# Optimization experiments

Hardware: AMD Instinct MI355X
Metric: run time of the kernel (lower is better)

The kernel has to match this reference:

```python
import jax, jax.numpy as jnp
import numpy as np

B, L, E, H = 2, 2048, 1024, 16
D = E // H

def setup_inputs() -> dict:
    key = jax.random.key(0)
    ks = jax.random.split(key, 6)
    values = jax.random.normal(ks[0], (B, L, E), dtype=jnp.float32)
    keys = jax.random.normal(ks[1], (B, L, E), dtype=jnp.float32)
    query = jax.random.normal(ks[2], (B, L, E), dtype=jnp.float32)
    mask = jax.random.randint(ks[3], (B, 1, L, L), 0, 2, dtype=jnp.int32)
    W_out = jax.random.normal(ks[4], (E, E), dtype=jnp.float32) * 0.02
    b_out = jax.random.normal(ks[5], (E,), dtype=jnp.float32) * 0.02
    return {"values": values, "keys": keys, "query": query, "mask": mask,
            "W_out": W_out, "b_out": b_out}

def reference(values, keys, query, mask, W_out, b_out):
    # Note: source module never applies its per-head q/k/v Linear layers;
    # it only reshapes inputs, so we do the same.
    b, l, e = query.shape
    v = values.reshape(b, l, H, D)   # [B, K, H, D]
    k = keys.reshape(b, l, H, D)     # [B, K, H, D]
    q = query.reshape(b, l, H, D)    # [B, Q, H, D]
    # scores[b,h,q,k] = sum_d q[b,q,h,d] * k[b,k,h,d]
    scores = jnp.einsum('bqhd,bkhd->bhqk', q, k)
    scores = jnp.where(mask == 0, jnp.float32(-1e20), scores)
    # source scales by 1/sqrt(embed_size), not head_dim
    attn = jax.nn.softmax(scores / jnp.float32(E ** 0.5), axis=3)
    out = jnp.einsum('bhqk,bkhd->bqhd', attn, v).reshape(b, l, e)
    out = out @ W_out.T + b_out  # torch Linear: x @ W^T + b
    return out
```

## Files before the change

kernel.cpp:

```cpp
#include <hip/hip_runtime.h>
#include <hip/hip_bf16.h>

typedef __bf16 bf16;
typedef __bf16 bf16x8 __attribute__((ext_vector_type(8)));
typedef __bf16 bf16x4 __attribute__((ext_vector_type(4)));
typedef float  f32x2  __attribute__((ext_vector_type(2)));
typedef float  f32x4  __attribute__((ext_vector_type(4)));
typedef float  f32x16 __attribute__((ext_vector_type(16)));

#define B_ 2
#define L_ 2048
#define E_ 1024
#define H_ 16
#define D_ 64

__device__ __forceinline__ int swz(int r, int c) {
    return r * 64 + (((c ^ (r & 7)) & 7) << 3);
}

#define DMA16(gp, lp)                                                              \
    __builtin_amdgcn_global_load_lds(                                              \
        (const __attribute__((address_space(1))) unsigned int*)(gp),               \
        (__attribute__((address_space(3))) unsigned int*)(lp), 16, 0, 0)

__global__ __launch_bounds__(256) void prep_kernel(const float* __restrict__ v,
                                                   const float* __restrict__ keys,
                                                   const int* __restrict__ mask,
                                                   const float* __restrict__ W,
                                                   bf16* __restrict__ vt_,
                                                   bf16* __restrict__ kt_,
                                                   unsigned int* __restrict__ mtq2,
                                                   bf16* __restrict__ wbt) {
    __shared__ __attribute__((aligned(16))) float tile[64 * 65];
    const int bid = blockIdx.x;
    const int t = threadIdx.x;
    if (bid < 1024) {
        int bh = bid >> 5, b = bh >> 4, h = bh & 15, kt = bid & 31;
        int kk = t >> 2, dg = t & 3;
        const float* src = v + (((size_t)(b * L_ + kt * 64 + kk)) * H_ + h) * D_ + dg * 16;
        float4 f[4];
#pragma unroll
        for (int i = 0; i < 4; i++) f[i] = reinterpret_cast<const float4*>(src)[i];
#pragma unroll
        for (int i = 0; i < 16; i++)
            tile[(dg * 16 + i) * 65 + kk] = reinterpret_cast<const float*>(f)[i];
        __syncthreads();
        int dd = t >> 2, cg = t & 3;
        const int sig[16] = {0, 1, 2, 3, 8, 9, 10, 11, 4, 5, 6, 7, 12, 13, 14, 15};
        bf16 tmp[16];
#pragma unroll
        for (int p = 0; p < 16; p++)
            tmp[p] = (bf16)tile[dd * 65 + cg * 16 + sig[p]];
        bf16* dst = vt_ + ((size_t)bh * 32 + kt) * 4096;
        *reinterpret_cast<uint4*>(dst + swz(dd, cg * 2))     = *reinterpret_cast<const uint4*>(&tmp[0]);
        *reinterpret_cast<uint4*>(dst + swz(dd, cg * 2 + 1)) = *reinterpret_cast<const uint4*>(&tmp[8]);
    } else if (bid < 2048) {
        int idx = bid - 1024;
        int b = idx >> 9;
        int q = (idx & 511) * 4 + (t >> 6);
        int li = t & 63;
        const int* mrow = mask + ((size_t)b * L_ + q) * L_;
        unsigned int* mq = mtq2 + (size_t)b * 64 * 2048;
#pragma unroll 2
        for (int pass = 0; pass < 8; pass++) {
            int4 m4 = reinterpret_cast<const int4*>(mrow)[pass * 64 + li];
            unsigned long long b0 = __ballot(m4.x & 1);
            unsigned long long b1 = __ballot(m4.y & 1);
            unsigned long long b2 = __ballot(m4.z & 1);
            unsigned long long b3 = __ballot(m4.w & 1);
            if (li < 8) {
                unsigned int word = (unsigned int)((b0 >> (8 * li)) & 0xFFull)
                                  | ((unsigned int)((b1 >> (8 * li)) & 0xFFull) << 8)
                                  | ((unsigned int)((b2 >> (8 * li)) & 0xFFull) << 16)
                                  | ((unsigned int)((b3 >> (8 * li)) & 0xFFull) << 24);
                mq[(size_t)(pass * 8 + li) * 2048 + q] = word;
            }
        }
    } else if (bid < 3072) {
        int idx = bid - 2048;
        int b = idx >> 9, h = (idx >> 5) & 15, kt = idx & 31;
        int r = t >> 2, cg = t & 3;
        const float* src = keys + ((size_t)(b * L_ + kt * 64 + r)) * E_ + h * 64 + cg * 16;
        float4 f[4];
#pragma unroll
        for (int i = 0; i < 4; i++) f[i] = reinterpret_cast<const float4*>(src)[i];
        bf16 tmp[16];
#pragma unroll
        for (int i = 0; i < 16; i++)
            tmp[i] = (bf16)reinterpret_cast<const float*>(f)[i];
        bf16* dst = kt_ + ((size_t)(b * 16 + h) * 32 + kt) * 4096;
        *reinterpret_cast<uint4*>(dst + swz(r, cg * 2))     = *reinterpret_cast<const uint4*>(&tmp[0]);
        *reinterpret_cast<uint4*>(dst + swz(r, cg * 2 + 1)) = *reinterpret_cast<const uint4*>(&tmp[8]);
    } else {
        int idx = bid - 3072;
        int n6 = idx >> 4, kt = idx & 15;
        int r = t >> 2, cg = t & 3;
        const float* src = W + ((size_t)(n6 * 64 + r)) * E_ + kt * 64 + cg * 16;
        float4 f[4];
#pragma unroll
        for (int i = 0; i < 4; i++) f[i] = reinterpret_cast<const float4*>(src)[i];
        bf16 tmp[16];
#pragma unroll
        for (int i = 0; i < 16; i++)
            tmp[i] = (bf16)reinterpret_cast<const float*>(f)[i];
        bf16* dst = wbt + ((size_t)(n6 * 16 + kt)) * 4096;
        *reinterpret_cast<uint4*>(dst + swz(r, cg * 2))     = *reinterpret_cast<const uint4*>(&tmp[0]);
        *reinterpret_cast<uint4*>(dst + swz(r, cg * 2 + 1)) = *reinterpret_cast<const uint4*>(&tmp[8]);
    }
}

__global__ __launch_bounds__(256, 4) void attn_kernel(const float* __restrict__ q_,
                                                      const bf16* __restrict__ kt_,
                                                      const bf16* __restrict__ vt_,
                                                      const unsigned int* __restrict__ mtq2,
                                                      bf16* __restrict__ xbt) {
    __shared__ __attribute__((aligned(16))) char smem[40960];
    bf16* Qs = (bf16*)(smem + 32768);
    float* Om = (float*)smem;
    float* Lrow = (float*)(smem + 16384);
    bf16* Xs = (bf16*)(smem + 16896);

    const int bh = blockIdx.y, b = bh >> 4, hd = bh & 15;
    const int q0 = blockIdx.x * 64;
    const int t = threadIdx.x;
    const int w = t >> 6, lane = t & 63, h = lane >> 5, l31 = lane & 31;
    const int wq = w & 1, wk = w >> 1;
    const int r_ = t >> 2, cg = t & 3;

    const float CSCALE = 1.4426950408889634f / 32.0f;

    const bf16* kbase = kt_ + (size_t)bh * 32 * 4096;
    const bf16* vbase = vt_ + (size_t)bh * 32 * 4096;

    {
        const bf16* gk = kbase + w * 1024 + lane * 8;
        DMA16(gk, smem + w * 2048);
        DMA16(gk + 512, smem + w * 2048 + 1024);
        const bf16* gv = vbase + w * 1024 + lane * 8;
        DMA16(gv, smem + 16384 + w * 2048);
        DMA16(gv + 512, smem + 16384 + w * 2048 + 1024);
    }
    {
        const float* src = q_ + ((size_t)(b * L_ + q0 + r_)) * E_ + hd * 64 + cg * 16;
        float4 f[4];
#pragma unroll
        for (int i = 0; i < 4; i++) f[i] = reinterpret_cast<const float4*>(src)[i];
        bf16 tmp[16];
#pragma unroll
        for (int i = 0; i < 16; i++)
            tmp[i] = (bf16)(reinterpret_cast<const float*>(f)[i] * CSCALE);
        *reinterpret_cast<uint4*>(&Qs[swz(r_, cg * 2)])     = *reinterpret_cast<const uint4*>(&tmp[0]);
        *reinterpret_cast<uint4*>(&Qs[swz(r_, cg * 2 + 1)]) = *reinterpret_cast<const uint4*>(&tmp[8]);
    }
    __syncthreads();

    bf16x8 bq[4];
#pragma unroll
    for (int dc = 0; dc < 4; dc++)
        bq[dc] = *reinterpret_cast<const bf16x8*>(&Qs[swz(wq * 32 + l31, dc * 2 + h)]);

    f32x16 oc[2] = {{}, {}};
    f32x2 ls = {0.0f, 0.0f};

    const unsigned int* mbase = mtq2 + (size_t)b * 64 * 2048 + q0 + wq * 32 + l31;
    unsigned int mw = mbase[(size_t)wk * 2048];

    for (int kt = 0; kt < L_ / 64; kt++) {
        __syncthreads();
        bf16* Kc = (bf16*)(smem + (kt & 1) * 8192);
        bf16* Vc = (bf16*)(smem + 16384 + (kt & 1) * 8192);
        if (kt + 1 < L_ / 64) {
            char* Kn = smem + ((kt + 1) & 1) * 8192;
            char* Vn = smem + 16384 + ((kt + 1) & 1) * 8192;
            const bf16* gk = kbase + (size_t)(kt + 1) * 4096 + w * 1024 + lane * 8;
            DMA16(gk, Kn + w * 2048);
            DMA16(gk + 512, Kn + w * 2048 + 1024);
            const bf16* gv = vbase + (size_t)(kt + 1) * 4096 + w * 1024 + lane * 8;
            DMA16(gv, Vn + w * 2048);
            DMA16(gv + 512, Vn + w * 2048 + 1024);
        }
        unsigned int mw_nxt = (kt + 1 < L_ / 64)
                                  ? mbase[(size_t)((kt + 1) * 2 + wk) * 2048] : 0u;

        f32x16 st = {};
        __builtin_amdgcn_s_setprio(1);
#pragma unroll
        for (int dc = 0; dc < 4; dc++) {
            bf16x8 ak = *reinterpret_cast<const bf16x8*>(&Kc[swz(wk * 32 + l31, dc * 2 + h)]);
            st = __builtin_amdgcn_mfma_f32_32x32x16_bf16(ak, bq[dc], st, 0, 0, 0);
        }
        __builtin_amdgcn_s_setprio(0);

        const unsigned int mwh = mw >> h;
        float pv[16];
#pragma unroll
        for (int i = 0; i < 16; i += 2) {
            const int b0 = 8 * (i & 3) + 2 * (i >> 2);
            const int b1 = 8 * ((i + 1) & 3) + 2 * ((i + 1) >> 2);
            float e0 = __builtin_amdgcn_exp2f(st[i]);
            float e1 = __builtin_amdgcn_exp2f(st[i + 1]);
            int m0 = ((int)(mwh << (31 - b0))) >> 31;
            int m1 = ((int)(mwh << (31 - b1))) >> 31;
            pv[i]     = __int_as_float(__float_as_int(e0) & m0);
            pv[i + 1] = __int_as_float(__float_as_int(e1) & m1);
            ls += (f32x2){pv[i], pv[i + 1]};
        }
        bf16x8 bp[2];
#pragma unroll
        for (int kc = 0; kc < 2; kc++)
#pragma unroll
            for (int j = 0; j < 8; j++)
                bp[kc][j] = (bf16)pv[kc * 8 + j];

        __builtin_amdgcn_s_setprio(1);
#pragma unroll
        for (int da = 0; da < 2; da++)
#pragma unroll
            for (int kc = 0; kc < 2; kc++) {
                bf16x8 av = *reinterpret_cast<const bf16x8*>(&Vc[swz(da * 32 + l31, wk * 4 + kc * 2 + h)]);
                oc[da] = __builtin_amdgcn_mfma_f32_32x32x16_bf16(av, bp[kc], oc[da], 0, 0, 0);
            }
        __builtin_amdgcn_s_setprio(0);
        mw = mw_nxt;
    }
    __syncthreads();

    float lsum = ls.x + ls.y;
    float lw = lsum + __shfl(lsum, lane ^ 32, 64);
    if (wk == 1) {
#pragma unroll
        for (int da = 0; da < 2; da++)
#pragma unroll
            for (int i = 0; i < 16; i++) {
                int d = da * 32 + (i & 3) + 8 * (i >> 2) + 4 * h;
                Om[d * 64 + wq * 32 + l31] = oc[da][i];
            }
        if (h == 0) Lrow[wq * 32 + l31] = lw;
    }
    __syncthreads();
    if (wk == 0) {
        float rinv = 1.0f / (lw + Lrow[wq * 32 + l31]);
#pragma unroll
        for (int da = 0; da < 2; da++)
#pragma unroll
            for (int g = 0; g < 4; g++) {
                int d0 = da * 32 + 8 * g + 4 * h;
                bf16x4 pk;
#pragma unroll
                for (int r = 0; r < 4; r++)
                    pk[r] = (bf16)((oc[da][g * 4 + r] + Om[(d0 + r) * 64 + wq * 32 + l31]) * rinv);
                *reinterpret_cast<bf16x4*>(&Xs[(wq * 32 + l31) * 72 + d0]) = pk;
            }
    }
    __syncthreads();
    {
        bf16* xtile = xbt + ((size_t)((b * 32 + (q0 >> 6)) * 16 + hd)) * 4096;
        *reinterpret_cast<uint4*>(xtile + swz(r_, cg * 2))     = *reinterpret_cast<const uint4*>(&Xs[r_ * 72 + cg * 16]);
        *reinterpret_cast<uint4*>(xtile + swz(r_, cg * 2 + 1)) = *reinterpret_cast<const uint4*>(&Xs[r_ * 72 + cg * 16 + 8]);
    }
}

__global__ __launch_bounds__(256, 3) void proj_kernel(const bf16* __restrict__ xbt,
                                                      const bf16* __restrict__ wbt,
                                                      const float* __restrict__ bias,
                                                      float* __restrict__ out) {
    __shared__ __attribute__((aligned(16))) char smem[49152];
    const int n0 = blockIdx.x * 64, m0 = blockIdx.y * 128;
    const int t = threadIdx.x;
    const int w = t >> 6, lane = t & 63, h = lane >> 5, l31 = lane & 31;
    const int wm = w >> 1, wn = w & 1;

    const bf16* a0 = xbt + ((size_t)(m0 >> 6)) * 16 * 4096;
    const bf16* a1 = a0 + 16 * 4096;
    const bf16* bb_ = wbt + ((size_t)(n0 >> 6)) * 16 * 4096;

    {
#pragma unroll
        for (int i = 0; i < 4; i++) {
            int c = w * 4 + i;
            const bf16* g = ((c >> 3) ? a1 : a0) + (c & 7) * 512 + lane * 8;
            DMA16(g, smem + c * 1024);
        }
#pragma unroll
        for (int i = 0; i < 2; i++) {
            int c = w * 2 + i;
            DMA16(bb_ + c * 512 + lane * 8, smem + 32768 + c * 1024);
        }
    }

    f32x16 acc[2] = {{}, {}};
    for (int kt = 0; kt < E_ / 64; kt++) {
        __syncthreads();
        bf16* Ac = (bf16*)(smem + (kt & 1) * 16384);
        bf16* Bc = (bf16*)(smem + 32768 + (kt & 1) * 8192);
        if (kt + 1 < E_ / 64) {
            char* An = smem + ((kt + 1) & 1) * 16384;
            char* Bn = smem + 32768 + ((kt + 1) & 1) * 8192;
            const bf16* an0 = a0 + (kt + 1) * 4096;
            const bf16* an1 = a1 + (kt + 1) * 4096;
            const bf16* bn = bb_ + (kt + 1) * 4096;
#pragma unroll
            for (int i = 0; i < 4; i++) {
                int c = w * 4 + i;
                const bf16* g = ((c >> 3) ? an1 : an0) + (c & 7) * 512 + lane * 8;
                DMA16(g, An + c * 1024);
            }
#pragma unroll
            for (int i = 0; i < 2; i++) {
                int c = w * 2 + i;
                DMA16(bn + c * 512 + lane * 8, Bn + c * 1024);
            }
        }
#pragma unroll
        for (int dc = 0; dc < 4; dc++) {
            bf16x8 bfr = *reinterpret_cast<const bf16x8*>(&Bc[swz(wn * 32 + l31, dc * 2 + h)]);
#pragma unroll
            for (int mi = 0; mi < 2; mi++) {
                bf16x8 afr = *reinterpret_cast<const bf16x8*>(&Ac[wm * 4096 + swz(mi * 32 + l31, dc * 2 + h)]);
                acc[mi] = __builtin_amdgcn_mfma_f32_32x32x16_bf16(afr, bfr, acc[mi], 0, 0, 0);
            }
        }
    }

    float bv = bias[n0 + wn * 32 + l31];
#pragma unroll
    for (int mi = 0; mi < 2; mi++)
#pragma unroll
        for (int i = 0; i < 16; i++) {
            int row = m0 + wm * 64 + mi * 32 + (i & 3) + 8 * (i >> 2) + 4 * h;
            out[(size_t)row * E_ + n0 + wn * 32 + l31] = acc[mi][i] + bv;
        }
}

extern "C" void kernel_launch(void* const* d_in, const int* in_sizes, int n_in,
                              void* d_out, int out_size, void* d_ws, size_t ws_size,
                              hipStream_t stream) {
    (void)in_sizes; (void)n_in; (void)out_size; (void)ws_size;
    const float* values = (const float*)d_in[0];
    const float* keys   = (const float*)d_in[1];
    const float* query  = (const float*)d_in[2];
    const int*   mask   = (const int*)d_in[3];
    const float* W_out  = (const float*)d_in[4];
    const float* b_out  = (const float*)d_in[5];
    float* out = (float*)d_out;

    char* ws = (char*)d_ws;
    bf16* vt_ = (bf16*)(ws);
    bf16* kt_ = (bf16*)(ws + 8388608);
    bf16* wbt = (bf16*)(ws + 16777216);
    unsigned int* mtq2 = (unsigned int*)(ws + 18874368);
    bf16* xbt = (bf16*)(ws + 19922944);

    prep_kernel<<<3328, 256, 0, stream>>>(values, keys, mask, W_out, vt_, kt_, mtq2, wbt);
    attn_kernel<<<dim3(L_ / 64, B_ * H_), 256, 0, stream>>>(query, kt_, vt_, mtq2, xbt);
    proj_kernel<<<dim3(E_ / 64, (B_ * L_) / 128), 256, 0, stream>>>(xbt, wbt, b_out, out);
}
```

Baseline: 191.6 us.

## Software-pipeline QK^T of the next tile with PV of the previous tile

Restructures the attention loop so each iteration issues the QK^T MFMAs for key tile kt together with the PV MFMAs for tile kt-1, with a peeled prologue and epilogue. V tiles move to triple buffering, reusing the Q staging area once Q is in registers. The goal is to hide the exp/mask/convert latency between the two matmuls behind independent MFMA work. The grid is also transposed so consecutive blocks cover different heads at the same query tile, which changes cache locality. The cost is more live registers (preloaded K and V fragments plus the carried score tile), which may pressure occupancy at the launch bound of 4.

```diff
diff --git a/kernel.cpp b/kernel.cpp
--- a/kernel.cpp
+++ b/kernel.cpp
@@ -120,8 +120,8 @@
     float* Lrow = (float*)(smem + 16384);
     bf16* Xs = (bf16*)(smem + 16896);
 
-    const int bh = blockIdx.y, b = bh >> 4, hd = bh & 15;
-    const int q0 = blockIdx.x * 64;
+    const int bh = blockIdx.x, b = bh >> 4, hd = bh & 15;
+    const int q0 = blockIdx.y * 64;
     const int t = threadIdx.x;
     const int w = t >> 6, lane = t & 63, h = lane >> 5, l31 = lane & 31;
     const int wq = w & 1, wk = w >> 1;
@@ -159,39 +159,59 @@
     for (int dc = 0; dc < 4; dc++)
         bq[dc] = *reinterpret_cast<const bf16x8*>(&Qs[swz(wq * 32 + l31, dc * 2 + h)]);
 
+    {
+        const bf16* gk = kbase + 4096 + w * 1024 + lane * 8;
+        DMA16(gk, smem + 8192 + w * 2048);
+        DMA16(gk + 512, smem + 8192 + w * 2048 + 1024);
+        const bf16* gv = vbase + 4096 + w * 1024 + lane * 8;
+        DMA16(gv, smem + 24576 + w * 2048);
+        DMA16(gv + 512, smem + 24576 + w * 2048 + 1024);
+    }
+
+    const unsigned int* mbase = mtq2 + (size_t)b * 64 * 2048 + q0 + wq * 32 + l31;
+    unsigned int mwHeld = mbase[(size_t)wk * 2048];
+
     f32x16 oc[2] = {{}, {}};
     f32x2 ls = {0.0f, 0.0f};
 
-    const unsigned int* mbase = mtq2 + (size_t)b * 64 * 2048 + q0 + wq * 32 + l31;
-    unsigned int mw = mbase[(size_t)wk * 2048];
-
-    for (int kt = 0; kt < L_ / 64; kt++) {
-        __syncthreads();
-        bf16* Kc = (bf16*)(smem + (kt & 1) * 8192);
-        bf16* Vc = (bf16*)(smem + 16384 + (kt & 1) * 8192);
-        if (kt + 1 < L_ / 64) {
-            char* Kn = smem + ((kt + 1) & 1) * 8192;
-            char* Vn = smem + 16384 + ((kt + 1) & 1) * 8192;
-            const bf16* gk = kbase + (size_t)(kt + 1) * 4096 + w * 1024 + lane * 8;
-            DMA16(gk, Kn + w * 2048);
-            DMA16(gk + 512, Kn + w * 2048 + 1024);
-            const bf16* gv = vbase + (size_t)(kt + 1) * 4096 + w * 1024 + lane * 8;
-            DMA16(gv, Vn + w * 2048);
-            DMA16(gv + 512, Vn + w * 2048 + 1024);
-        }
-        unsigned int mw_nxt = (kt + 1 < L_ / 64)
-                                  ? mbase[(size_t)((kt + 1) * 2 + wk) * 2048] : 0u;
-
-        f32x16 st = {};
-        __builtin_amdgcn_s_setprio(1);
+    f32x16 st = {};
+    {
+        const bf16* Kc = (const bf16*)smem;
 #pragma unroll
         for (int dc = 0; dc < 4; dc++) {
             bf16x8 ak = *reinterpret_cast<const bf16x8*>(&Kc[swz(wk * 32 + l31, dc * 2 + h)]);
             st = __builtin_amdgcn_mfma_f32_32x32x16_bf16(ak, bq[dc], st, 0, 0, 0);
         }
-        __builtin_amdgcn_s_setprio(0);
-
-        const unsigned int mwh = mw >> h;
+    }
+
+    int vP = 16384, vC = 24576, vN = 32768;
+    for (int kt = 1; kt < L_ / 64; kt++) {
+        __syncthreads();
+        const int koff = (kt & 1) << 13;
+        if (kt + 1 < L_ / 64) {
+            const int koffN = koff ^ 8192;
+            const bf16* gk = kbase + (size_t)(kt + 1) * 4096 + w * 1024 + lane * 8;
+            DMA16(gk, smem + koffN + w * 2048);
+            DMA16(gk + 512, smem + koffN + w * 2048 + 1024);
+            const bf16* gv = vbase + (size_t)(kt + 1) * 4096 + w * 1024 + lane * 8;
+            DMA16(gv, smem + vN + w * 2048);
+            DMA16(gv + 512, smem + vN + w * 2048 + 1024);
+        }
+        unsigned int mwN = mbase[(size_t)(kt * 2 + wk) * 2048];
+
+        const bf16* Kc = (const bf16*)(smem + koff);
+        const bf16* Vp = (const bf16*)(smem + vP);
+        bf16x8 ak[4], av[4];
+#pragma unroll
+        for (int dc = 0; dc < 4; dc++)
+            ak[dc] = *reinterpret_cast<const bf16x8*>(&Kc[swz(wk * 32 + l31, dc * 2 + h)]);
+#pragma unroll
+        for (int j = 0; j < 4; j++) {
+            const int da = j >> 1, kc = j & 1;
+            av[j] = *reinterpret_cast<const bf16x8*>(&Vp[swz(da * 32 + l31, wk * 4 + kc * 2 + h)]);
+        }
+
+        const unsigned int mwh = mwHeld >> h;
         float pv[16];
 #pragma unroll
         for (int i = 0; i < 16; i += 2) {
@@ -213,15 +233,49 @@
                 bp[kc][j] = (bf16)pv[kc * 8 + j];
 
         __builtin_amdgcn_s_setprio(1);
-#pragma unroll
-        for (int da = 0; da < 2; da++)
-#pragma unroll
-            for (int kc = 0; kc < 2; kc++) {
-                bf16x8 av = *reinterpret_cast<const bf16x8*>(&Vc[swz(da * 32 + l31, wk * 4 + kc * 2 + h)]);
-                oc[da] = __builtin_amdgcn_mfma_f32_32x32x16_bf16(av, bp[kc], oc[da], 0, 0, 0);
-            }
+        st = (f32x16){};
+#pragma unroll
+        for (int dc = 0; dc < 4; dc++)
+            st = __builtin_amdgcn_mfma_f32_32x32x16_bf16(ak[dc], bq[dc], st, 0, 0, 0);
+#pragma unroll
+        for (int j = 0; j < 4; j++) {
+            const int da = j >> 1, kc = j & 1;
+            oc[da] = __builtin_amdgcn_mfma_f32_32x32x16_bf16(av[j], bp[kc], oc[da], 0, 0, 0);
+        }
         __builtin_amdgcn_s_setprio(0);
-        mw = mw_nxt;
+
+        mwHeld = mwN;
+        int tmpv = vP; vP = vC; vC = vN; vN = tmpv;
+    }
+
+    {
+        const unsigned int mwh = mwHeld >> h;
+        float pv[16];
+#pragma unroll
+        for (int i = 0; i < 16; i += 2) {
+            const int b0 = 8 * (i & 3) + 2 * (i >> 2);
+            const int b1 = 8 * ((i + 1) & 3) + 2 * ((i + 1) >> 2);
+            float e0 = __builtin_amdgcn_exp2f(st[i]);
+            float e1 = __builtin_amdgcn_exp2f(st[i + 1]);
+            int m0 = ((int)(mwh << (31 - b0))) >> 31;
+            int m1 = ((int)(mwh << (31 - b1))) >> 31;
+            pv[i]     = __int_as_float(__float_as_int(e0) & m0);
+            pv[i + 1] = __int_as_float(__float_as_int(e1) & m1);
+            ls += (f32x2){pv[i], pv[i + 1]};
+        }
+        bf16x8 bp[2];
+#pragma unroll
+        for (int kc = 0; kc < 2; kc++)
+#pragma unroll
+            for (int j = 0; j < 8; j++)
+                bp[kc][j] = (bf16)pv[kc * 8 + j];
+        const bf16* Vp = (const bf16*)(smem + vP);
+#pragma unroll
+        for (int j = 0; j < 4; j++) {
+            const int da = j >> 1, kc = j & 1;
+            bf16x8 av = *reinterpret_cast<const bf16x8*>(&Vp[swz(da * 32 + l31, wk * 4 + kc * 2 + h)]);
+            oc[da] = __builtin_amdgcn_mfma_f32_32x32x16_bf16(av, bp[kc], oc[da], 0, 0, 0);
+        }
     }
     __syncthreads();
 
@@ -352,6 +406,6 @@
     bf16* xbt = (bf16*)(ws + 19922944);
 
     prep_kernel<<<3328, 256, 0, stream>>>(values, keys, mask, W_out, vt_, kt_, mtq2, wbt);
-    attn_kernel<<<dim3(L_ / 64, B_ * H_), 256, 0, stream>>>(query, kt_, vt_, mtq2, xbt);
+    attn_kernel<<<dim3(B_ * H_, L_ / 64), 256, 0, stream>>>(query, kt_, vt_, mtq2, xbt);
     proj_kernel<<<dim3(E_ / 64, (B_ * L_) / 128), 256, 0, stream>>>(xbt, wbt, b_out, out);
 }
```

Result: no change. 195.3 us (+1.9%).

## Halve attention block to two waves, each covering all 64 queries

Applied to the files above, without the earlier changes.

The attention kernel now runs with 128 threads (2 waves) instead of 4. Each wave handles one 32-key half of every tile for all 64 queries. K and V fragments are loaded from LDS once per tile and reused across two query halves, which doubles the MFMA work per LDS read and halves the waves that sync on each barrier. The mask word is now loaded in the same iteration rather than prefetched. The cost is roughly twice the accumulator registers per wave and fewer waves per block to hide latency.

```diff
diff --git a/kernel.cpp b/kernel.cpp
--- a/kernel.cpp
+++ b/kernel.cpp
@@ -109,7 +109,7 @@
     }
 }
 
-__global__ __launch_bounds__(256, 4) void attn_kernel(const float* __restrict__ q_,
+__global__ __launch_bounds__(128, 2) void attn_kernel(const float* __restrict__ q_,
                                                       const bf16* __restrict__ kt_,
                                                       const bf16* __restrict__ vt_,
                                                       const unsigned int* __restrict__ mtq2,
@@ -124,8 +124,7 @@
     const int q0 = blockIdx.x * 64;
     const int t = threadIdx.x;
     const int w = t >> 6, lane = t & 63, h = lane >> 5, l31 = lane & 31;
-    const int wq = w & 1, wk = w >> 1;
-    const int r_ = t >> 2, cg = t & 3;
+    const int r_ = t >> 1, half = t & 1;
 
     const float CSCALE = 1.4426950408889634f / 32.0f;
 
@@ -133,130 +132,163 @@
     const bf16* vbase = vt_ + (size_t)bh * 32 * 4096;
 
     {
-        const bf16* gk = kbase + w * 1024 + lane * 8;
-        DMA16(gk, smem + w * 2048);
-        DMA16(gk + 512, smem + w * 2048 + 1024);
-        const bf16* gv = vbase + w * 1024 + lane * 8;
-        DMA16(gv, smem + 16384 + w * 2048);
-        DMA16(gv + 512, smem + 16384 + w * 2048 + 1024);
+        const bf16* gk = kbase + w * 2048 + lane * 8;
+        const bf16* gv = vbase + w * 2048 + lane * 8;
+#pragma unroll
+        for (int i = 0; i < 4; i++) {
+            DMA16(gk + i * 512, smem + w * 4096 + i * 1024);
+            DMA16(gv + i * 512, smem + 16384 + w * 4096 + i * 1024);
+        }
     }
     {
-        const float* src = q_ + ((size_t)(b * L_ + q0 + r_)) * E_ + hd * 64 + cg * 16;
-        float4 f[4];
-#pragma unroll
-        for (int i = 0; i < 4; i++) f[i] = reinterpret_cast<const float4*>(src)[i];
-        bf16 tmp[16];
-#pragma unroll
-        for (int i = 0; i < 16; i++)
+        const float* src = q_ + ((size_t)(b * L_ + q0 + r_)) * E_ + hd * 64 + half * 32;
+        float4 f[8];
+#pragma unroll
+        for (int i = 0; i < 8; i++) f[i] = reinterpret_cast<const float4*>(src)[i];
+        bf16 tmp[32];
+#pragma unroll
+        for (int i = 0; i < 32; i++)
             tmp[i] = (bf16)(reinterpret_cast<const float*>(f)[i] * CSCALE);
-        *reinterpret_cast<uint4*>(&Qs[swz(r_, cg * 2)])     = *reinterpret_cast<const uint4*>(&tmp[0]);
-        *reinterpret_cast<uint4*>(&Qs[swz(r_, cg * 2 + 1)]) = *reinterpret_cast<const uint4*>(&tmp[8]);
+#pragma unroll
+        for (int j = 0; j < 4; j++)
+            *reinterpret_cast<uint4*>(&Qs[swz(r_, half * 4 + j)]) =
+                *reinterpret_cast<const uint4*>(&tmp[j * 8]);
     }
     __syncthreads();
 
-    bf16x8 bq[4];
-#pragma unroll
-    for (int dc = 0; dc < 4; dc++)
-        bq[dc] = *reinterpret_cast<const bf16x8*>(&Qs[swz(wq * 32 + l31, dc * 2 + h)]);
-
-    f32x16 oc[2] = {{}, {}};
-    f32x2 ls = {0.0f, 0.0f};
-
-    const unsigned int* mbase = mtq2 + (size_t)b * 64 * 2048 + q0 + wq * 32 + l31;
-    unsigned int mw = mbase[(size_t)wk * 2048];
+    bf16x8 bq[2][4];
+#pragma unroll
+    for (int qh = 0; qh < 2; qh++)
+#pragma unroll
+        for (int dc = 0; dc < 4; dc++)
+            bq[qh][dc] = *reinterpret_cast<const bf16x8*>(&Qs[swz(qh * 32 + l31, dc * 2 + h)]);
+
+    f32x16 oc[2][2] = {{{}, {}}, {{}, {}}};
+    f32x2 ls[2] = {{0.0f, 0.0f}, {0.0f, 0.0f}};
+
+    const unsigned int* mbase = mtq2 + (size_t)b * 64 * 2048 + q0 + l31;
 
     for (int kt = 0; kt < L_ / 64; kt++) {
         __syncthreads();
-        bf16* Kc = (bf16*)(smem + (kt & 1) * 8192);
-        bf16* Vc = (bf16*)(smem + 16384 + (kt & 1) * 8192);
+        const bf16* Kc = (const bf16*)(smem + (kt & 1) * 8192);
+        const bf16* Vc = (const bf16*)(smem + 16384 + (kt & 1) * 8192);
         if (kt + 1 < L_ / 64) {
-            char* Kn = smem + ((kt + 1) & 1) * 8192;
-            char* Vn = smem + 16384 + ((kt + 1) & 1) * 8192;
-            const bf16* gk = kbase + (size_t)(kt + 1) * 4096 + w * 1024 + lane * 8;
-            DMA16(gk, Kn + w * 2048);
-            DMA16(gk + 512, Kn + w * 2048 + 1024);
-            const bf16* gv = vbase + (size_t)(kt + 1) * 4096 + w * 1024 + lane * 8;
-            DMA16(gv, Vn + w * 2048);
-            DMA16(gv + 512, Vn + w * 2048 + 1024);
-        }
-        unsigned int mw_nxt = (kt + 1 < L_ / 64)
-                                  ? mbase[(size_t)((kt + 1) * 2 + wk) * 2048] : 0u;
-
-        f32x16 st = {};
+            char* Kn = smem + ((kt + 1) & 1) * 8192 + w * 4096;
+            char* Vn = smem + 16384 + ((kt + 1) & 1) * 8192 + w * 4096;
+            const bf16* gk = kbase + (size_t)(kt + 1) * 4096 + w * 2048 + lane * 8;
+            const bf16* gv = vbase + (size_t)(kt + 1) * 4096 + w * 2048 + lane * 8;
+#pragma unroll
+            for (int i = 0; i < 4; i++) {
+                DMA16(gk + i * 512, Kn + i * 1024);
+                DMA16(gv + i * 512, Vn + i * 1024);
+            }
+        }
+        unsigned int mw0 = mbase[(size_t)(kt * 2 + w) * 2048];
+        unsigned int mw1 = mbase[(size_t)(kt * 2 + w) * 2048 + 32];
+
+        bf16x8 ak[4], av[4];
+#pragma unroll
+        for (int dc = 0; dc < 4; dc++)
+            ak[dc] = *reinterpret_cast<const bf16x8*>(&Kc[swz(w * 32 + l31, dc * 2 + h)]);
+#pragma unroll
+        for (int j = 0; j < 4; j++) {
+            const int da = j >> 1, kc = j & 1;
+            av[j] = *reinterpret_cast<const bf16x8*>(&Vc[swz(da * 32 + l31, w * 4 + kc * 2 + h)]);
+        }
+
+        f32x16 st[2] = {{}, {}};
         __builtin_amdgcn_s_setprio(1);
 #pragma unroll
         for (int dc = 0; dc < 4; dc++) {
-            bf16x8 ak = *reinterpret_cast<const bf16x8*>(&Kc[swz(wk * 32 + l31, dc * 2 + h)]);
-            st = __builtin_amdgcn_mfma_f32_32x32x16_bf16(ak, bq[dc], st, 0, 0, 0);
+            st[0] = __builtin_amdgcn_mfma_f32_32x32x16_bf16(ak[dc], bq[0][dc], st[0], 0, 0, 0);
+            st[1] = __builtin_amdgcn_mfma_f32_32x32x16_bf16(ak[dc], bq[1][dc], st[1], 0, 0, 0);
         }
         __builtin_amdgcn_s_setprio(0);
 
-        const unsigned int mwh = mw >> h;
-        float pv[16];
-#pragma unroll
-        for (int i = 0; i < 16; i += 2) {
-            const int b0 = 8 * (i & 3) + 2 * (i >> 2);
-            const int b1 = 8 * ((i + 1) & 3) + 2 * ((i + 1) >> 2);
-            float e0 = __builtin_amdgcn_exp2f(st[i]);
-            float e1 = __builtin_amdgcn_exp2f(st[i + 1]);
-            int m0 = ((int)(mwh << (31 - b0))) >> 31;
-            int m1 = ((int)(mwh << (31 - b1))) >> 31;
-            pv[i]     = __int_as_float(__float_as_int(e0) & m0);
-            pv[i + 1] = __int_as_float(__float_as_int(e1) & m1);
-            ls += (f32x2){pv[i], pv[i + 1]};
-        }
-        bf16x8 bp[2];
-#pragma unroll
-        for (int kc = 0; kc < 2; kc++)
-#pragma unroll
-            for (int j = 0; j < 8; j++)
-                bp[kc][j] = (bf16)pv[kc * 8 + j];
+        bf16x8 bp[2][2];
+#pragma unroll
+        for (int qh = 0; qh < 2; qh++) {
+            const unsigned int mwh = (qh ? mw1 : mw0) >> h;
+            float pv[16];
+#pragma unroll
+            for (int i = 0; i < 16; i += 2) {
+                const int b0 = 8 * (i & 3) + 2 * (i >> 2);
+                const int b1 = 8 * ((i + 1) & 3) + 2 * ((i + 1) >> 2);
+                float e0 = __builtin_amdgcn_exp2f(st[qh][i]);
+                float e1 = __builtin_amdgcn_exp2f(st[qh][i + 1]);
+                int m0 = ((int)(mwh << (31 - b0))) >> 31;
+                int m1 = ((int)(mwh << (31 - b1))) >> 31;
+                pv[i]     = __int_as_float(__float_as_int(e0) & m0);
+                pv[i + 1] = __int_as_float(__float_as_int(e1) & m1);
+                ls[qh] += (f32x2){pv[i], pv[i + 1]};
+            }
+#pragma unroll
+            for (int kc = 0; kc < 2; kc++)
+#pragma unroll
+                for (int j = 0; j < 8; j++)
+                    bp[qh][kc][j] = (bf16)pv[kc * 8 + j];
+        }
 
         __builtin_amdgcn_s_setprio(1);
 #pragma unroll
         for (int da = 0; da < 2; da++)
 #pragma unroll
             for (int kc = 0; kc < 2; kc++) {
-                bf16x8 av = *reinterpret_cast<const bf16x8*>(&Vc[swz(da * 32 + l31, wk * 4 + kc * 2 + h)]);
-                oc[da] = __builtin_amdgcn_mfma_f32_32x32x16_bf16(av, bp[kc], oc[da], 0, 0, 0);
+                oc[0][da] = __builtin_amdgcn_mfma_f32_32x32x16_bf16(av[da * 2 + kc], bp[0][kc], oc[0][da], 0, 0, 0);
+                oc[1][da] = __builtin_amdgcn_mfma_f32_32x32x16_bf16(av[da * 2 + kc], bp[1][kc], oc[1][da], 0, 0, 0);
             }
         __builtin_amdgcn_s_setprio(0);
-        mw = mw_nxt;
     }
     __syncthreads();
 
-    float lsum = ls.x + ls.y;
-    float lw = lsum + __shfl(lsum, lane ^ 32, 64);
-    if (wk == 1) {
-#pragma unroll
-        for (int da = 0; da < 2; da++)
-#pragma unroll
-            for (int i = 0; i < 16; i++) {
-                int d = da * 32 + (i & 3) + 8 * (i >> 2) + 4 * h;
-                Om[d * 64 + wq * 32 + l31] = oc[da][i];
-            }
-        if (h == 0) Lrow[wq * 32 + l31] = lw;
+    float lw[2];
+#pragma unroll
+    for (int qh = 0; qh < 2; qh++) {
+        float s = ls[qh].x + ls[qh].y;
+        lw[qh] = s + __shfl(s, lane ^ 32, 64);
+    }
+    if (w == 1) {
+#pragma unroll
+        for (int qh = 0; qh < 2; qh++)
+#pragma unroll
+            for (int da = 0; da < 2; da++)
+#pragma unroll
+                for (int i = 0; i < 16; i++) {
+                    int d = da * 32 + (i & 3) + 8 * (i >> 2) + 4 * h;
+                    Om[d * 64 + qh * 32 + l31] = oc[qh][da][i];
+                }
+        if (h == 0) {
+            Lrow[l31] = lw[0];
+            Lrow[32 + l31] = lw[1];
+        }
     }
     __syncthreads();
-    if (wk == 0) {
-        float rinv = 1.0f / (lw + Lrow[wq * 32 + l31]);
-#pragma unroll
-        for (int da = 0; da < 2; da++)
-#pragma unroll
-            for (int g = 0; g < 4; g++) {
-                int d0 = da * 32 + 8 * g + 4 * h;
-                bf16x4 pk;
-#pragma unroll
-                for (int r = 0; r < 4; r++)
-                    pk[r] = (bf16)((oc[da][g * 4 + r] + Om[(d0 + r) * 64 + wq * 32 + l31]) * rinv);
-                *reinterpret_cast<bf16x4*>(&Xs[(wq * 32 + l31) * 72 + d0]) = pk;
-            }
+    if (w == 0) {
+#pragma unroll
+        for (int qh = 0; qh < 2; qh++) {
+            float rinv = 1.0f / (lw[qh] + Lrow[qh * 32 + l31]);
+#pragma unroll
+            for (int da = 0; da < 2; da++)
+#pragma unroll
+                for (int g = 0; g < 4; g++) {
+                    int d0 = da * 32 + 8 * g + 4 * h;
+                    bf16x4 pk;
+#pragma unroll
+                    for (int r = 0; r < 4; r++)
+                        pk[r] = (bf16)((oc[qh][da][g * 4 + r] + Om[(d0 + r) * 64 + qh * 32 + l31]) * rinv);
+                    *reinterpret_cast<bf16x4*>(&Xs[(qh * 32 + l31) * 72 + d0]) = pk;
+                }
+        }
     }
     __syncthreads();
     {
         bf16* xtile = xbt + ((size_t)((b * 32 + (q0 >> 6)) * 16 + hd)) * 4096;
-        *reinterpret_cast<uint4*>(xtile + swz(r_, cg * 2))     = *reinterpret_cast<const uint4*>(&Xs[r_ * 72 + cg * 16]);
-        *reinterpret_cast<uint4*>(xtile + swz(r_, cg * 2 + 1)) = *reinterpret_cast<const uint4*>(&Xs[r_ * 72 + cg * 16 + 8]);
+#pragma unroll
+        for (int j = 0; j < 4; j++) {
+            int c = half * 4 + j;
+            *reinterpret_cast<uint4*>(xtile + swz(r_, c)) =
+                *reinterpret_cast<const uint4*>(&Xs[r_ * 72 + c * 8]);
+        }
     }
 }
 
@@ -352,6 +384,6 @@
     bf16* xbt = (bf16*)(ws + 19922944);
 
     prep_kernel<<<3328, 256, 0, stream>>>(values, keys, mask, W_out, vt_, kt_, mtq2, wbt);
-    attn_kernel<<<dim3(L_ / 64, B_ * H_), 256, 0, stream>>>(query, kt_, vt_, mtq2, xbt);
+    attn_kernel<<<dim3(L_ / 64, B_ * H_), 128, 0, stream>>>(query, kt_, vt_, mtq2, xbt);
     proj_kernel<<<dim3(E_ / 64, (B_ * L_) / 128), 256, 0, stream>>>(xbt, wbt, b_out, out);
 }
```

Result: no change. 193.7 us (+1.1%).

## Apply mask as additive bf16 bias via MFMA instead of bitmask ANDs

Applied to the files above, without the earlier changes.

Replaces the packed bitmask with a bf16 bias tile (0 or -512) laid out per 64x64 q/k block. The attention kernel streams these tiles into LDS alongside K/V and adds them to the scores with two extra MFMAs against an identity-like operand, which removes the per-element shift/AND masking in the softmax loop. In exchange the mask tensor in the workspace grows by a factor of 16. Each head reloads the mask tile every iteration, and an extra barrier is added per iteration. exp2(-512) underflows to zero, so masked entries are dropped only approximately.

```diff
diff --git a/kernel.cpp b/kernel.cpp
--- a/kernel.cpp
+++ b/kernel.cpp
@@ -29,7 +29,7 @@
                                                    const float* __restrict__ W,
                                                    bf16* __restrict__ vt_,
                                                    bf16* __restrict__ kt_,
-                                                   unsigned int* __restrict__ mtq2,
+                                                   bf16* __restrict__ mbt,
                                                    bf16* __restrict__ wbt) {
     __shared__ __attribute__((aligned(16))) float tile[64 * 65];
     const int bid = blockIdx.x;
@@ -54,30 +54,30 @@
         bf16* dst = vt_ + ((size_t)bh * 32 + kt) * 4096;
         *reinterpret_cast<uint4*>(dst + swz(dd, cg * 2))     = *reinterpret_cast<const uint4*>(&tmp[0]);
         *reinterpret_cast<uint4*>(dst + swz(dd, cg * 2 + 1)) = *reinterpret_cast<const uint4*>(&tmp[8]);
-    } else if (bid < 2048) {
+    } else if (bid < 3072) {
         int idx = bid - 1024;
-        int b = idx >> 9;
-        int q = (idx & 511) * 4 + (t >> 6);
-        int li = t & 63;
-        const int* mrow = mask + ((size_t)b * L_ + q) * L_;
-        unsigned int* mq = mtq2 + (size_t)b * 64 * 2048;
-#pragma unroll 2
-        for (int pass = 0; pass < 8; pass++) {
-            int4 m4 = reinterpret_cast<const int4*>(mrow)[pass * 64 + li];
-            unsigned long long b0 = __ballot(m4.x & 1);
-            unsigned long long b1 = __ballot(m4.y & 1);
-            unsigned long long b2 = __ballot(m4.z & 1);
-            unsigned long long b3 = __ballot(m4.w & 1);
-            if (li < 8) {
-                unsigned int word = (unsigned int)((b0 >> (8 * li)) & 0xFFull)
-                                  | ((unsigned int)((b1 >> (8 * li)) & 0xFFull) << 8)
-                                  | ((unsigned int)((b2 >> (8 * li)) & 0xFFull) << 16)
-                                  | ((unsigned int)((b3 >> (8 * li)) & 0xFFull) << 24);
-                mq[(size_t)(pass * 8 + li) * 2048 + q] = word;
-            }
-        }
-    } else if (bid < 3072) {
-        int idx = bid - 2048;
+        int b = idx >> 10, qt = (idx >> 5) & 31, kt = idx & 31;
+        unsigned short* Lt = (unsigned short*)tile;
+        int q = t >> 2, kc = t & 3;
+        const int* mrow = mask + ((size_t)b * L_ + qt * 64 + q) * L_ + kt * 64 + kc * 16;
+        int4 m4[4];
+#pragma unroll
+        for (int i = 0; i < 4; i++) m4[i] = reinterpret_cast<const int4*>(mrow)[i];
+#pragma unroll
+        for (int i = 0; i < 16; i++)
+            Lt[(kc * 16 + i) * 72 + q] =
+                (reinterpret_cast<const int*>(m4)[i] & 1) ? (unsigned short)0x0000
+                                                          : (unsigned short)0xC400;
+        __syncthreads();
+        int r = t >> 2, cg = t & 3;
+        unsigned short tmp[16];
+#pragma unroll
+        for (int i = 0; i < 16; i++) tmp[i] = Lt[r * 72 + cg * 16 + i];
+        bf16* dst = mbt + ((size_t)((b * 32 + qt) * 32) + kt) * 4096;
+        *reinterpret_cast<uint4*>(dst + swz(r, cg * 2))     = *reinterpret_cast<const uint4*>(&tmp[0]);
+        *reinterpret_cast<uint4*>(dst + swz(r, cg * 2 + 1)) = *reinterpret_cast<const uint4*>(&tmp[8]);
+    } else if (bid < 4096) {
+        int idx = bid - 3072;
         int b = idx >> 9, h = (idx >> 5) & 15, kt = idx & 31;
         int r = t >> 2, cg = t & 3;
         const float* src = keys + ((size_t)(b * L_ + kt * 64 + r)) * E_ + h * 64 + cg * 16;
@@ -92,7 +92,7 @@
         *reinterpret_cast<uint4*>(dst + swz(r, cg * 2))     = *reinterpret_cast<const uint4*>(&tmp[0]);
         *reinterpret_cast<uint4*>(dst + swz(r, cg * 2 + 1)) = *reinterpret_cast<const uint4*>(&tmp[8]);
     } else {
-        int idx = bid - 3072;
+        int idx = bid - 4096;
         int n6 = idx >> 4, kt = idx & 15;
         int r = t >> 2, cg = t & 3;
         const float* src = W + ((size_t)(n6 * 64 + r)) * E_ + kt * 64 + cg * 16;
@@ -112,7 +112,7 @@
 __global__ __launch_bounds__(256, 4) void attn_kernel(const float* __restrict__ q_,
                                                       const bf16* __restrict__ kt_,
                                                       const bf16* __restrict__ vt_,
-                                                      const unsigned int* __restrict__ mtq2,
+                                                      const bf16* __restrict__ mbt,
                                                       bf16* __restrict__ xbt) {
     __shared__ __attribute__((aligned(16))) char smem[40960];
     bf16* Qs = (bf16*)(smem + 32768);
@@ -131,6 +131,7 @@
 
     const bf16* kbase = kt_ + (size_t)bh * 32 * 4096;
     const bf16* vbase = vt_ + (size_t)bh * 32 * 4096;
+    const bf16* mbase = mbt + (size_t)((b * 32 + (q0 >> 6)) * 32) * 4096;
 
     {
         const bf16* gk = kbase + w * 1024 + lane * 8;
@@ -158,17 +159,43 @@
 #pragma unroll
     for (int dc = 0; dc < 4; dc++)
         bq[dc] = *reinterpret_cast<const bf16x8*>(&Qs[swz(wq * 32 + l31, dc * 2 + h)]);
+    __syncthreads();
+
+    {
+        const bf16* gm = mbase + w * 1024 + lane * 8;
+        DMA16(gm, smem + 32768 + w * 2048);
+        DMA16(gm + 512, smem + 32768 + w * 2048 + 1024);
+    }
+
+    bf16x8 bi0, bi1;
+    {
+        const int i0 = l31 - h * 8;
+        uint u0 = (i0 == 0) ? 0x00003F80u : (i0 == 1) ? 0x3F800000u : 0u;
+        uint u1 = (i0 == 2) ? 0x00003F80u : (i0 == 3) ? 0x3F800000u : 0u;
+        uint u2 = (i0 == 4) ? 0x00003F80u : (i0 == 5) ? 0x3F800000u : 0u;
+        uint u3 = (i0 == 6) ? 0x00003F80u : (i0 == 7) ? 0x3F800000u : 0u;
+        uint4 uu = {u0, u1, u2, u3};
+        bi0 = *reinterpret_cast<bf16x8*>(&uu);
+        const int i1 = l31 - 16 - h * 8;
+        u0 = (i1 == 0) ? 0x00003F80u : (i1 == 1) ? 0x3F800000u : 0u;
+        u1 = (i1 == 2) ? 0x00003F80u : (i1 == 3) ? 0x3F800000u : 0u;
+        u2 = (i1 == 4) ? 0x00003F80u : (i1 == 5) ? 0x3F800000u : 0u;
+        u3 = (i1 == 6) ? 0x00003F80u : (i1 == 7) ? 0x3F800000u : 0u;
+        uint4 uu1 = {u0, u1, u2, u3};
+        bi1 = *reinterpret_cast<bf16x8*>(&uu1);
+    }
 
     f32x16 oc[2] = {{}, {}};
     f32x2 ls = {0.0f, 0.0f};
 
-    const unsigned int* mbase = mtq2 + (size_t)b * 64 * 2048 + q0 + wq * 32 + l31;
-    unsigned int mw = mbase[(size_t)wk * 2048];
-
     for (int kt = 0; kt < L_ / 64; kt++) {
         __syncthreads();
-        bf16* Kc = (bf16*)(smem + (kt & 1) * 8192);
-        bf16* Vc = (bf16*)(smem + 16384 + (kt & 1) * 8192);
+        const bf16* Kc = (const bf16*)(smem + (kt & 1) * 8192);
+        const bf16* Vc = (const bf16*)(smem + 16384 + (kt & 1) * 8192);
+        const bf16* Mc = (const bf16*)(smem + 32768);
+        bf16x8 am0 = *reinterpret_cast<const bf16x8*>(&Mc[swz(wk * 32 + l31, wq * 4 + 0 + h)]);
+        bf16x8 am1 = *reinterpret_cast<const bf16x8*>(&Mc[swz(wk * 32 + l31, wq * 4 + 2 + h)]);
+        __syncthreads();
         if (kt + 1 < L_ / 64) {
             char* Kn = smem + ((kt + 1) & 1) * 8192;
             char* Vn = smem + 16384 + ((kt + 1) & 1) * 8192;
@@ -178,12 +205,15 @@
             const bf16* gv = vbase + (size_t)(kt + 1) * 4096 + w * 1024 + lane * 8;
             DMA16(gv, Vn + w * 2048);
             DMA16(gv + 512, Vn + w * 2048 + 1024);
-        }
-        unsigned int mw_nxt = (kt + 1 < L_ / 64)
-                                  ? mbase[(size_t)((kt + 1) * 2 + wk) * 2048] : 0u;
+            const bf16* gm = mbase + (size_t)(kt + 1) * 4096 + w * 1024 + lane * 8;
+            DMA16(gm, smem + 32768 + w * 2048);
+            DMA16(gm + 512, smem + 32768 + w * 2048 + 1024);
+        }
 
         f32x16 st = {};
         __builtin_amdgcn_s_setprio(1);
+        st = __builtin_amdgcn_mfma_f32_32x32x16_bf16(am0, bi0, st, 0, 0, 0);
+        st = __builtin_amdgcn_mfma_f32_32x32x16_bf16(am1, bi1, st, 0, 0, 0);
 #pragma unroll
         for (int dc = 0; dc < 4; dc++) {
             bf16x8 ak = *reinterpret_cast<const bf16x8*>(&Kc[swz(wk * 32 + l31, dc * 2 + h)]);
@@ -191,26 +221,15 @@
         }
         __builtin_amdgcn_s_setprio(0);
 
-        const unsigned int mwh = mw >> h;
-        float pv[16];
+        bf16x8 bp[2];
 #pragma unroll
         for (int i = 0; i < 16; i += 2) {
-            const int b0 = 8 * (i & 3) + 2 * (i >> 2);
-            const int b1 = 8 * ((i + 1) & 3) + 2 * ((i + 1) >> 2);
             float e0 = __builtin_amdgcn_exp2f(st[i]);
             float e1 = __builtin_amdgcn_exp2f(st[i + 1]);
-            int m0 = ((int)(mwh << (31 - b0))) >> 31;
-            int m1 = ((int)(mwh << (31 - b1))) >> 31;
-            pv[i]     = __int_as_float(__float_as_int(e0) & m0);
-            pv[i + 1] = __int_as_float(__float_as_int(e1) & m1);
-            ls += (f32x2){pv[i], pv[i + 1]};
-        }
-        bf16x8 bp[2];
-#pragma unroll
-        for (int kc = 0; kc < 2; kc++)
-#pragma unroll
-            for (int j = 0; j < 8; j++)
-                bp[kc][j] = (bf16)pv[kc * 8 + j];
+            ls += (f32x2){e0, e1};
+            bp[i >> 3][i & 7] = (bf16)e0;
+            bp[(i + 1) >> 3][(i + 1) & 7] = (bf16)e1;
+        }
 
         __builtin_amdgcn_s_setprio(1);
 #pragma unroll
@@ -221,7 +240,6 @@
                 oc[da] = __builtin_amdgcn_mfma_f32_32x32x16_bf16(av, bp[kc], oc[da], 0, 0, 0);
             }
         __builtin_amdgcn_s_setprio(0);
-        mw = mw_nxt;
     }
     __syncthreads();
 
@@ -348,10 +366,10 @@
     bf16* vt_ = (bf16*)(ws);
     bf16* kt_ = (bf16*)(ws + 8388608);
     bf16* wbt = (bf16*)(ws + 16777216);
-    unsigned int* mtq2 = (unsigned int*)(ws + 18874368);
-    bf16* xbt = (bf16*)(ws + 19922944);
-
-    prep_kernel<<<3328, 256, 0, stream>>>(values, keys, mask, W_out, vt_, kt_, mtq2, wbt);
-    attn_kernel<<<dim3(L_ / 64, B_ * H_), 256, 0, stream>>>(query, kt_, vt_, mtq2, xbt);
+    bf16* mbt = (bf16*)(ws + 18874368);
+    bf16* xbt = (bf16*)(ws + 35651584);
+
+    prep_kernel<<<4352, 256, 0, stream>>>(values, keys, mask, W_out, vt_, kt_, mbt, wbt);
+    attn_kernel<<<dim3(L_ / 64, B_ * H_), 256, 0, stream>>>(query, kt_, vt_, mbt, xbt);
     proj_kernel<<<dim3(E_ / 64, (B_ * L_) / 128), 256, 0, stream>>>(xbt, wbt, b_out, out);
 }
```

Result: no change. 191.7 us (+0.0%).
